# Performance work log

Hardware: AMD Instinct MI355X
Metric: run time of the kernel (lower is better)

Reference implementation:

```python
import math
import jax, jax.numpy as jnp
import numpy as np

DIM = 768
TARGET_DIM = 1024  # next power of two >= DIM


def _hadamard_matrix(n: int) -> np.ndarray:
    # Sylvester construction, normalized by 1/sqrt(n)
    H = np.array([[1.0]], dtype=np.float32)
    while H.shape[0] < n:
        H = np.block([[H, H], [H, -H]])
    return H / math.sqrt(n)


_H = jnp.asarray(_hadamard_matrix(TARGET_DIM))  # [1024, 1024]


def setup_inputs() -> dict:
    key = jax.random.key(0)
    x = jax.random.normal(key, (16, 768, 56, 56), dtype=jnp.float32)
    return {"x": x}


def reference(x):
    B, C, Hs, Ws = x.shape  # C == DIM
    # [B, C, H, W] -> [B, H, W, C] -> [B*H*W, C]
    xr = jnp.transpose(x, (0, 2, 3, 1)).reshape(-1, DIM)
    # pad channel dim up to TARGET_DIM
    xp = jnp.pad(xr, ((0, 0), (0, TARGET_DIM - DIM)))
    y = xp @ _H.astype(x.dtype)           # [B*H*W, 1024]
    y = y[:, :DIM]                        # slice back to dim
    y = y.reshape(B, Hs, Ws, C)
    return jnp.transpose(y, (0, 3, 1, 2))  # [B, C, H, W]
```

## Files before the change

kernel.cpp:

```cpp
#include <hip/hip_runtime.h>


#define NSPAT 3136
#define TS    32
#define STQ   33
#define STI   529

static __device__ __forceinline__ float2 f2add(float2 a, float2 b) {
    return make_float2(a.x + b.x, a.y + b.y);
}
static __device__ __forceinline__ float2 f2sub(float2 a, float2 b) {
    return make_float2(a.x - b.x, a.y - b.y);
}

#define FWHT_STAGE2(arr, D)                                  \
    _Pragma("unroll")                                        \
    for (int _b = 0; _b < 32; _b += 2 * (D)) {               \
        _Pragma("unroll")                                    \
        for (int _k = 0; _k < (D); ++_k) {                   \
            float2 _t = arr[_b + _k];                        \
            arr[_b + _k]       = f2add(_t, arr[_b + _k + (D)]); \
            arr[_b + _k + (D)] = f2sub(_t, arr[_b + _k + (D)]); \
        }                                                    \
    }

#define FWHT32_2(arr)      \
    FWHT_STAGE2(arr, 16)   \
    FWHT_STAGE2(arr, 8)    \
    FWHT_STAGE2(arr, 4)    \
    FWHT_STAGE2(arr, 2)    \
    FWHT_STAGE2(arr, 1)

#define FWHT_STAGE1(arr, D)                                  \
    _Pragma("unroll")                                        \
    for (int _b = 0; _b < 32; _b += 2 * (D)) {               \
        _Pragma("unroll")                                    \
        for (int _k = 0; _k < (D); ++_k) {                   \
            float _t = arr[_b + _k];                         \
            arr[_b + _k]       = _t + arr[_b + _k + (D)];    \
            arr[_b + _k + (D)] = _t - arr[_b + _k + (D)];    \
        }                                                    \
    }

__global__ __launch_bounds__(512, 5)
void hadamard_c768_kernel(const float* __restrict__ x, float* __restrict__ y) {
    __shared__ float lds[24 * STI];

    const int t   = threadIdx.x;
    const int bid = blockIdx.x;
    const int b   = bid / (NSPAT / TS);
    const int s0  = (bid % (NSPAT / TS)) * TS;
    const int base = b * 768 * NSPAT + s0;

    const int g  = t >> 4;
    const int ln = t & 15;

    float2 a[32];
    const bool active = (g < 24);
    if (active) {
        const float* xb = x + base + 2 * ln;
        #pragma unroll
        for (int j = 0; j < 32; ++j)
            a[j] = *(const float2*)(xb + (32 * g + j) * NSPAT);
        FWHT32_2(a)
    }

    const int q16 = t >> 5;
    const int s   = t & 31;

    #pragma unroll
    for (int r = 0; r < 2; ++r) {
        if (active) {
            float* p = lds + g * STI + 2 * ln;
            #pragma unroll
            for (int qq = 0; qq < 16; ++qq) {
                p[qq * STQ]     = a[16 * r + qq].x;
                p[qq * STQ + 1] = a[16 * r + qq].y;
            }
        }
        __syncthreads();

        {
            float w[32];
            const float* p = lds + q16 * STQ + s;
            #pragma unroll
            for (int i = 0; i < 24; ++i)
                w[i] = p[i * STI];

            #pragma unroll
            for (int i = 0; i < 8; ++i) {
                float tt  = w[i];
                w[i]      = tt + w[i + 16];
                w[i + 16] = tt - w[i + 16];
            }
            #pragma unroll
            for (int i = 8; i < 16; ++i)
                w[i + 16] = w[i];

            FWHT_STAGE1(w, 8)
            FWHT_STAGE1(w, 4)
            FWHT_STAGE1(w, 2)
            FWHT_STAGE1(w, 1)

            const int q = 16 * r + q16;
            float* yb = y + base + s;
            #pragma unroll
            for (int pp = 0; pp < 24; ++pp)
                __builtin_nontemporal_store(w[pp] * 0.03125f,
                                            yb + (32 * pp + q) * NSPAT);
        }
        if (r == 0)
            __syncthreads();
    }
}

extern "C" void kernel_launch(void* const* d_in, const int* in_sizes, int n_in,
                              void* d_out, int out_size, void* d_ws, size_t ws_size,
                              hipStream_t stream) {
    const float* x = (const float*)d_in[0];
    float*       y = (float*)d_out;
    const int nblocks = 16 * (NSPAT / TS);
    hadamard_c768_kernel<<<dim3(nblocks), dim3(512), 0, stream>>>(x, y);
}
```

Measured before the change: 267.7 us.

## Use 768 threads with one spatial column per thread and split transpose phases

Replaces the 512-thread block (384 active threads, each loading float2 pairs) with 768 threads, each loading one float per channel across 32 channels. The second FWHT stage now runs in two phases: 24 q-rows for all threads, then the remaining 8 q-rows, where each thread writes a subset of the output channels. LDS stride changes to fit the wider layout. The goal is to put all threads to work and raise memory-level parallelism, at the cost of more redundant work in the second phase, an extra barrier, and scalar rather than float2 loads.

Measured after the change: 312.9 us. 16.9% more time.

```diff
diff --git a/kernel.cpp b/kernel.cpp
--- a/kernel.cpp
+++ b/kernel.cpp
@@ -4,32 +4,7 @@
 #define NSPAT 3136
 #define TS    32
 #define STQ   33
-#define STI   529
-
-static __device__ __forceinline__ float2 f2add(float2 a, float2 b) {
-    return make_float2(a.x + b.x, a.y + b.y);
-}
-static __device__ __forceinline__ float2 f2sub(float2 a, float2 b) {
-    return make_float2(a.x - b.x, a.y - b.y);
-}
-
-#define FWHT_STAGE2(arr, D)                                  \
-    _Pragma("unroll")                                        \
-    for (int _b = 0; _b < 32; _b += 2 * (D)) {               \
-        _Pragma("unroll")                                    \
-        for (int _k = 0; _k < (D); ++_k) {                   \
-            float2 _t = arr[_b + _k];                        \
-            arr[_b + _k]       = f2add(_t, arr[_b + _k + (D)]); \
-            arr[_b + _k + (D)] = f2sub(_t, arr[_b + _k + (D)]); \
-        }                                                    \
-    }
-
-#define FWHT32_2(arr)      \
-    FWHT_STAGE2(arr, 16)   \
-    FWHT_STAGE2(arr, 8)    \
-    FWHT_STAGE2(arr, 4)    \
-    FWHT_STAGE2(arr, 2)    \
-    FWHT_STAGE2(arr, 1)
+#define STI   793
 
 #define FWHT_STAGE1(arr, D)                                  \
     _Pragma("unroll")                                        \
@@ -42,7 +17,14 @@
         }                                                    \
     }
 
-__global__ __launch_bounds__(512, 5)
+#define FWHT32_1(arr)      \
+    FWHT_STAGE1(arr, 16)   \
+    FWHT_STAGE1(arr, 8)    \
+    FWHT_STAGE1(arr, 4)    \
+    FWHT_STAGE1(arr, 2)    \
+    FWHT_STAGE1(arr, 1)
+
+__global__ __launch_bounds__(768, 6)
 void hadamard_c768_kernel(const float* __restrict__ x, float* __restrict__ y) {
     __shared__ float lds[24 * STI];
 
@@ -52,65 +34,96 @@
     const int s0  = (bid % (NSPAT / TS)) * TS;
     const int base = b * 768 * NSPAT + s0;
 
-    const int g  = t >> 4;
-    const int ln = t & 15;
+    const int g  = t >> 5;
+    const int ln = t & 31;
 
-    float2 a[32];
-    const bool active = (g < 24);
-    if (active) {
-        const float* xb = x + base + 2 * ln;
+    float a[32];
+    {
+        const float* xb = x + base + ln;
         #pragma unroll
         for (int j = 0; j < 32; ++j)
-            a[j] = *(const float2*)(xb + (32 * g + j) * NSPAT);
-        FWHT32_2(a)
+            a[j] = xb[(32 * g + j) * NSPAT];
+        FWHT32_1(a)
     }
 
-    const int q16 = t >> 5;
-    const int s   = t & 31;
+    {
+        float* p = lds + g * STI + ln;
+        #pragma unroll
+        for (int q = 0; q < 24; ++q)
+            p[q * STQ] = a[q];
+    }
+    __syncthreads();
 
-    #pragma unroll
-    for (int r = 0; r < 2; ++r) {
-        if (active) {
-            float* p = lds + g * STI + 2 * ln;
-            #pragma unroll
-            for (int qq = 0; qq < 16; ++qq) {
-                p[qq * STQ]     = a[16 * r + qq].x;
-                p[qq * STQ + 1] = a[16 * r + qq].y;
-            }
+    float w[32];
+    {
+        const float* p = lds + g * STQ + ln;
+        #pragma unroll
+        for (int i = 0; i < 24; ++i)
+            w[i] = p[i * STI];
+    }
+    __syncthreads();
+
+    {
+        float* p = lds + g * STI + ln;
+        #pragma unroll
+        for (int q = 0; q < 8; ++q)
+            p[q * STQ] = a[24 + q];
+    }
+
+    {
+        #pragma unroll
+        for (int i = 0; i < 8; ++i) {
+            float tt  = w[i];
+            w[i]      = tt + w[i + 16];
+            w[i + 16] = tt - w[i + 16];
         }
-        __syncthreads();
+        #pragma unroll
+        for (int i = 8; i < 16; ++i)
+            w[i + 16] = w[i];
 
-        {
-            float w[32];
-            const float* p = lds + q16 * STQ + s;
-            #pragma unroll
-            for (int i = 0; i < 24; ++i)
-                w[i] = p[i * STI];
+        FWHT_STAGE1(w, 8)
+        FWHT_STAGE1(w, 4)
+        FWHT_STAGE1(w, 2)
+        FWHT_STAGE1(w, 1)
 
-            #pragma unroll
-            for (int i = 0; i < 8; ++i) {
-                float tt  = w[i];
-                w[i]      = tt + w[i + 16];
-                w[i + 16] = tt - w[i + 16];
-            }
-            #pragma unroll
-            for (int i = 8; i < 16; ++i)
-                w[i + 16] = w[i];
+        float* yb = y + base + ln;
+        #pragma unroll
+        for (int pp = 0; pp < 24; ++pp)
+            __builtin_nontemporal_store(w[pp] * 0.03125f,
+                                        yb + (32 * pp + g) * NSPAT);
+    }
+    __syncthreads();
 
-            FWHT_STAGE1(w, 8)
-            FWHT_STAGE1(w, 4)
-            FWHT_STAGE1(w, 2)
-            FWHT_STAGE1(w, 1)
+    {
+        const int q8    = g & 7;
+        const int pbase = (g >> 3) * 8;
+        const float* p  = lds + q8 * STQ + ln;
 
-            const int q = 16 * r + q16;
-            float* yb = y + base + s;
-            #pragma unroll
-            for (int pp = 0; pp < 24; ++pp)
-                __builtin_nontemporal_store(w[pp] * 0.03125f,
-                                            yb + (32 * pp + q) * NSPAT);
+        #pragma unroll
+        for (int i = 0; i < 24; ++i)
+            w[i] = p[i * STI];
+
+        #pragma unroll
+        for (int i = 0; i < 8; ++i) {
+            float tt  = w[i];
+            w[i]      = tt + w[i + 16];
+            w[i + 16] = tt - w[i + 16];
         }
-        if (r == 0)
-            __syncthreads();
+        #pragma unroll
+        for (int i = 8; i < 16; ++i)
+            w[i + 16] = w[i];
+
+        FWHT_STAGE1(w, 8)
+        FWHT_STAGE1(w, 4)
+        FWHT_STAGE1(w, 2)
+        FWHT_STAGE1(w, 1)
+
+        const int q = 24 + q8;
+        float* yb = y + base + ln;
+        #pragma unroll
+        for (int pp = 0; pp < 8; ++pp)
+            __builtin_nontemporal_store(w[pbase + pp] * 0.03125f,
+                                        yb + (32 * (pbase + pp) + q) * NSPAT);
     }
 }
 
@@ -120,5 +133,5 @@
     const float* x = (const float*)d_in[0];
     float*       y = (float*)d_out;
     const int nblocks = 16 * (NSPAT / TS);
-    hadamard_c768_kernel<<<dim3(nblocks), dim3(512), 0, stream>>>(x, y);
+    hadamard_c768_kernel<<<dim3(nblocks), dim3(768), 0, stream>>>(x, y);
 }
```
